# Kernel optimization log

Hardware: AMD Instinct MI355X
Metric: run time of the kernel (lower is better)

The kernel has to match this reference:

```python
import jax, jax.numpy as jnp
import numpy as np

N = 30000   # nodes
E = 480000  # edges
IN = 128    # hidden_dim (in_feats)
H = 4       # num_heads
D = 128     # out_feats per head
HD = H * D
NEG_SLOPE = 0.2
BN_EPS = 1e-5


def setup_inputs() -> dict:
    key = jax.random.key(0)
    ks = jax.random.split(key, 12)
    feat = jax.random.normal(ks[0], (N, IN), dtype=jnp.float32)
    src = jax.random.randint(ks[1], (E,), 0, N)
    dst = jax.random.randint(ks[2], (E,), 0, N)
    sc_in = 1.0 / np.sqrt(IN)
    sc_hd = 1.0 / np.sqrt(HD)
    W_fc = jax.random.normal(ks[3], (IN, HD), dtype=jnp.float32) * sc_in
    attn_l = jax.random.normal(ks[4], (H, D), dtype=jnp.float32) * sc_in
    attn_r = jax.random.normal(ks[5], (H, D), dtype=jnp.float32) * sc_in
    W_res = jax.random.normal(ks[6], (IN, HD), dtype=jnp.float32) * sc_in
    bias_gat = jnp.zeros((HD,), dtype=jnp.float32)
    gamma = jnp.ones((HD,), dtype=jnp.float32)
    beta = jnp.zeros((HD,), dtype=jnp.float32)
    W_out = jax.random.normal(ks[7], (HD, IN), dtype=jnp.float32) * sc_hd
    b_out = jnp.zeros((IN,), dtype=jnp.float32)
    return dict(feat=feat, src=src, dst=dst, W_fc=W_fc, attn_l=attn_l,
                attn_r=attn_r, W_res=W_res, bias_gat=bias_gat,
                gamma=gamma, beta=beta, W_out=W_out, b_out=b_out)


def reference(feat, src, dst, W_fc, attn_l, attn_r, W_res, bias_gat,
              gamma, beta, W_out, b_out):
    # --- GATConv (eval mode: dropout off) ---
    h = (feat @ W_fc).reshape(N, H, D)               # projected feats [N,H,D]
    el = jnp.einsum('nhd,hd->nh', h, attn_l)         # [N,H]
    er = jnp.einsum('nhd,hd->nh', h, attn_r)         # [N,H]
    e = el[src] + er[dst]                            # [E,H]
    e = jnp.where(e > 0, e, NEG_SLOPE * e)           # leaky_relu(0.2)
    # segment softmax over edges grouped by destination node
    emax = jax.ops.segment_max(e, dst, num_segments=N)   # [N,H]
    emax = jnp.where(jnp.isfinite(emax), emax, 0.0)      # empty segments
    ex = jnp.exp(e - emax[dst])                          # [E,H]
    denom = jax.ops.segment_sum(ex, dst, num_segments=N) # [N,H]
    a = ex / denom[dst]                                  # [E,H] attention
    msgs = h[src] * a[:, :, None]                        # [E,H,D]
    rst = jax.ops.segment_sum(msgs, dst, num_segments=N) # [N,H,D]
    # residual (in_feats != H*out_feats -> linear res_fc) + bias
    rst = rst + (feat @ W_res).reshape(N, H, D) + bias_gat.reshape(1, H, D)
    # --- fc_out: Flatten -> BatchNorm1d (train stats) -> ReLU -> Linear ---
    x = rst.reshape(N, HD)
    mu = x.mean(axis=0)
    var = x.var(axis=0)
    xn = (x - mu) / jnp.sqrt(var + BN_EPS)
    x = jnp.maximum(gamma * xn + beta, 0.0)
    return x @ W_out + b_out                             # [N, IN]
```

## Files before the change

### kernel.cpp

```cpp
#include <hip/hip_runtime.h>

#define N_  30000
#define E_  480000

typedef short short8 __attribute__((ext_vector_type(8)));
typedef float f32x4  __attribute__((ext_vector_type(4)));
typedef float f32x2  __attribute__((ext_vector_type(2)));
typedef unsigned int u32x4 __attribute__((ext_vector_type(4)));
typedef unsigned int u32x2 __attribute__((ext_vector_type(2)));
typedef int i32x4 __attribute__((ext_vector_type(4)));
union Frag { u32x4 q; short8 v; unsigned short us[8]; };

__device__ __forceinline__ float b2f(unsigned short u){
  union { unsigned int i; float f; } v; v.i = ((unsigned int)u) << 16; return v.f;
}
__device__ __forceinline__ float blo(unsigned int u){
  union { unsigned int i; float f; } v; v.i = u << 16; return v.f;
}
__device__ __forceinline__ float bhi(unsigned int u){
  union { unsigned int i; float f; } v; v.i = u & 0xffff0000u; return v.f;
}
__device__ __forceinline__ unsigned short f2b(float f){
  union { float f; unsigned int u; } v; v.f = f;
  unsigned int u = v.u;
  return (unsigned short)((u + 0x7fffu + ((u >> 16) & 1u)) >> 16);
}

__global__ void k_initconv(const float* __restrict__ Wfc, const float* __restrict__ Wres,
                           const float* __restrict__ Wout,
                           const float* __restrict__ al, const float* __restrict__ ar,
                           unsigned short* __restrict__ Wt2, unsigned short* __restrict__ WtOut,
                           float* __restrict__ P,
                           int* __restrict__ counts, int* __restrict__ cursor){
  int bx = blockIdx.x;
  if (bx >= 256){
    int idx = (bx - 256) * 256 + threadIdx.x;
    if (idx < 1024){
      int k = idx >> 3, q = idx & 7;
      int h = q & 3;
      const float* a = (q < 4) ? al : ar;
      const float* wr = Wfc + k * 512 + h * 128;
      const float* av = a + h * 128;
      float s = 0.f;
#pragma unroll 4
      for (int d = 0; d < 128; d++) s += wr[d] * av[d];
      P[k * 8 + q] = s;
    }
    return;
  }
  int gid = bx * 256 + threadIdx.x;
  const int stride = 256 * 256;
  if (gid < N_){ counts[gid] = 0; cursor[gid] = 0; }
  const int total1 = 512 * 256;
  const int total2 = 128 * 512;
  for (int i = gid; i < total1 + total2; i += stride){
    if (i < total1){
      int c = i >> 8, k = i & 255;
      float v = (k < 128) ? Wfc[k * 512 + c] : Wres[(k - 128) * 512 + c];
      Wt2[((k >> 7) << 16) + c * 128 + (k & 127)] = f2b(v);
    } else {
      int j = i - total1;
      int n = j >> 9, k = j & 511;
      WtOut[((k >> 7) << 14) + n * 128 + (k & 127)] = f2b(Wout[k * 128 + n]);
    }
  }
}

__global__ __launch_bounds__(256) void k_el(const float* __restrict__ feat,
                                            const float* __restrict__ P,
                                            float* __restrict__ el, float* __restrict__ er,
                                            unsigned short* __restrict__ featb){
  __shared__ float sF[32 * 132];
  __shared__ float sP[1024];
  int t = threadIdx.x;
  int n0 = blockIdx.x * 32;
  *reinterpret_cast<f32x4*>(&sP[t * 4]) = *reinterpret_cast<const f32x4*>(P + t * 4);
#pragma unroll
  for (int i = 0; i < 4; i++){
    int c = t + i * 256;
    int r = c >> 5, cw = (c & 31) * 4;
    int gn = n0 + r;
    f32x4 v = {0.f, 0.f, 0.f, 0.f};
    if (gn < N_) v = *reinterpret_cast<const f32x4*>(feat + gn * 128 + cw);
    *reinterpret_cast<f32x4*>(&sF[r * 132 + cw]) = v;
  }
  __syncthreads();
#pragma unroll
  for (int i = 0; i < 8; i++){
    int c = t + i * 256;
    int r = c >> 6, cw = (c & 63) * 2;
    int gn = n0 + r;
    if (gn < N_){
      float v0 = sF[r * 132 + cw], v1 = sF[r * 132 + cw + 1];
      unsigned int pv = (unsigned int)f2b(v0) | ((unsigned int)f2b(v1) << 16);
      *reinterpret_cast<unsigned int*>(featb + gn * 128 + cw) = pv;
    }
  }
  int node = t >> 3, q = t & 7;
  int gn = n0 + node;
  const float* fr = &sF[node * 132];
  float s = 0.f;
#pragma unroll 2
  for (int k = 0; k < 128; k += 4){
    f32x4 fv = *reinterpret_cast<const f32x4*>(fr + k);
#pragma unroll
    for (int j = 0; j < 4; j++) s += fv[j] * sP[(k + j) * 8 + q];
  }
  if (gn < N_){
    if (q < 4) el[gn * 4 + q] = s;
    else       er[gn * 4 + (q - 4)] = s;
  }
}

__global__ void k_hist(const int* __restrict__ dst, int* __restrict__ counts){
  int e = blockIdx.x * 256 + threadIdx.x;
  if (e < E_) atomicAdd(&counts[dst[e]], 1);
}

__global__ __launch_bounds__(1024) void k_scan(const int* __restrict__ counts,
                                               int* __restrict__ offs){
  __shared__ int wsum[16];
  int t = threadIdx.x;
  int lane = t & 63, w = t >> 6;
  int base = t * 32;
  int vals[32];
  int s = 0;
  bool inb = (base < N_);
#pragma unroll
  for (int jj = 0; jj < 8; jj++){
    i32x4 cv = {0, 0, 0, 0};
    if (inb) cv = *reinterpret_cast<const i32x4*>(counts + base + jj * 4);
#pragma unroll
    for (int m = 0; m < 4; m++){
      int idx = base + jj * 4 + m;
      int v = (idx < N_) ? cv[m] : 0;
      vals[jj * 4 + m] = s;
      s += v;
    }
  }
  int x = s;
  for (int o = 1; o < 64; o <<= 1){
    int y = __shfl_up(x, o);
    if (lane >= o) x += y;
  }
  if (lane == 63) wsum[w] = x;
  __syncthreads();
  if (t < 16){
    int y = wsum[t];
    for (int o = 1; o < 16; o <<= 1){
      int z = __shfl_up(y, o, 16);
      if (t >= o) y += z;
    }
    wsum[t] = y;
  }
  __syncthreads();
  int wbase = (w > 0) ? wsum[w - 1] : 0;
  int ex = wbase + x - s;
#pragma unroll
  for (int j = 0; j < 32; j++){
    int idx = base + j;
    if (idx <= N_) offs[idx] = ex + vals[j];
  }
}

__global__ void k_edge(const int* __restrict__ src, const int* __restrict__ dst,
                       const float* __restrict__ el, const float* __restrict__ er,
                       float* __restrict__ ws_s, int* __restrict__ src_s,
                       const int* __restrict__ offs, int* __restrict__ cursor){
  int e = blockIdx.x * 256 + threadIdx.x;
  if (e >= E_) return;
  int s = src[e], d = dst[e];
  f32x4 a = *reinterpret_cast<const f32x4*>(el + s * 4);
  f32x4 b = *reinterpret_cast<const f32x4*>(er + d * 4);
  f32x4 v;
#pragma unroll
  for (int i = 0; i < 4; i++){
    float x = a[i] + b[i];
    x = x > 0.f ? x : 0.2f * x;
    v[i] = __expf(x);
  }
  int p = atomicAdd(&cursor[d], 1);
  int pos = offs[d] + p;
  *reinterpret_cast<f32x4*>(ws_s + pos * 4) = v;
  src_s[pos] = s;
}

__global__ __launch_bounds__(256) void k_aggrf(const int* __restrict__ offs,
                                               const int* __restrict__ src_s,
                                               const float* __restrict__ ws_s,
                                               const unsigned short* __restrict__ featb,
                                               unsigned short* __restrict__ fagg){
  int wave = threadIdx.x >> 6, lane = threadIdx.x & 63;
  int n = blockIdx.x * 4 + wave;
  if (n >= N_) return;
  int off0 = __builtin_amdgcn_readfirstlane(offs[n]);
  int g    = __builtin_amdgcn_readfirstlane(offs[n + 1]) - off0;
  int c0 = lane * 2;
  f32x2 acc2[4] = {};
  f32x4 wsum = {0.f, 0.f, 0.f, 0.f};

  auto FMA1 = [&](const f32x4& wv, unsigned int pv){
    wsum += wv;
    f32x2 lh; lh[0] = blo(pv); lh[1] = bhi(pv);
#pragma unroll
    for (int h = 0; h < 4; h++) acc2[h] += lh * wv[h];
  };

  int i = 0;
  while (i < g){
    int blk = g - i; if (blk > 64) blk = 64;
    int idx = i + lane;
    int ssrc = (idx < g) ? src_s[off0 + idx] : 0;
    int nfull = blk >> 3;
    if (nfull){
      int sa[8]; unsigned int pa[8]; f32x4 wa[8];
#pragma unroll
      for (int u = 0; u < 8; u++) sa[u] = __shfl(ssrc, u);
#pragma unroll
      for (int u = 0; u < 8; u++) pa[u] = *reinterpret_cast<const unsigned int*>(featb + sa[u] * 128 + c0);
#pragma unroll
      for (int u = 0; u < 8; u++) wa[u] = *reinterpret_cast<const f32x4*>(ws_s + (off0 + i + u) * 4);
      for (int c = 1; c < nfull; c++){
        int sb[8]; unsigned int pb[8]; f32x4 wb[8];
#pragma unroll
        for (int u = 0; u < 8; u++) sb[u] = __shfl(ssrc, c * 8 + u);
#pragma unroll
        for (int u = 0; u < 8; u++) pb[u] = *reinterpret_cast<const unsigned int*>(featb + sb[u] * 128 + c0);
#pragma unroll
        for (int u = 0; u < 8; u++) wb[u] = *reinterpret_cast<const f32x4*>(ws_s + (off0 + i + c * 8 + u) * 4);
#pragma unroll
        for (int u = 0; u < 8; u++) FMA1(wa[u], pa[u]);
#pragma unroll
        for (int u = 0; u < 8; u++){ pa[u] = pb[u]; wa[u] = wb[u]; }
      }
#pragma unroll
      for (int u = 0; u < 8; u++) FMA1(wa[u], pa[u]);
    }
    for (int j = nfull * 8; j < blk; j++){
      int s = __shfl(ssrc, j);
      unsigned int pv = *reinterpret_cast<const unsigned int*>(featb + s * 128 + c0);
      f32x4 wv = *reinterpret_cast<const f32x4*>(ws_s + (off0 + i + j) * 4);
      FMA1(wv, pv);
    }
    i += blk;
  }

  f32x4 rd;
#pragma unroll
  for (int h = 0; h < 4; h++) rd[h] = (wsum[h] > 0.f) ? 1.0f / wsum[h] : 0.f;
#pragma unroll
  for (int h = 0; h < 4; h++){
    unsigned int ov = (unsigned int)f2b(acc2[h][0] * rd[h]) |
                      ((unsigned int)f2b(acc2[h][1] * rd[h]) << 16);
    *reinterpret_cast<unsigned int*>(fagg + n * 512 + h * 128 + c0) = ov;
  }
}

__global__ __launch_bounds__(512) void k_gemmC(const unsigned short* __restrict__ fagg,
                                               const unsigned short* __restrict__ featb,
                                               const unsigned short* __restrict__ Wt2,
                                               const float* __restrict__ bias,
                                               unsigned short* __restrict__ comb,
                                               float* __restrict__ psum,
                                               float* __restrict__ psq){
  __shared__ unsigned short wsl[256 * 128];
  char* wb = (char*)wsl;
  int tid = threadIdx.x;
  int wave = tid >> 6, lane = tid & 63;
  int lrow = lane & 15, quad = lane >> 4;
  int rowbase = blockIdx.x * 128 + wave * 16;
  int colbase = blockIdx.y * 256;
  int h0 = blockIdx.y * 2;
  int arow = rowbase + lrow; if (arow > N_ - 1) arow = N_ - 1;
  const unsigned short* aF = fagg + arow * 512 + h0 * 128;
  const unsigned short* aX = featb + arow * 128;
  f32x4 acc[16] = {};
  for (int phase = 0; phase < 2; phase++){
    __syncthreads();
#pragma unroll
    for (int i = 0; i < 8; i++){
      int c = tid + i * 512;
      int col = c >> 4, unit = c & 15;
      u32x4 v = *reinterpret_cast<const u32x4*>(Wt2 + (phase << 16) + (colbase + col) * 128 + unit * 8);
      int byte = (col * 256 + unit * 16) ^ ((col & 7) << 4);
      *reinterpret_cast<u32x4*>(wb + byte) = v;
    }
    __syncthreads();
#pragma unroll
    for (int kk = 0; kk < 4; kk++){
      Frag a0, a1;
      if (phase == 0){
        a0.q = *reinterpret_cast<const u32x4*>(aF + kk * 32 + quad * 8);
        a1.q = *reinterpret_cast<const u32x4*>(aF + 128 + kk * 32 + quad * 8);
      } else {
        a0.q = *reinterpret_cast<const u32x4*>(aX + kk * 32 + quad * 8);
        a1.q = a0.q;
      }
#pragma unroll
      for (int s = 0; s < 16; s++){
        int r = s * 16 + lrow;
        int byte = (r * 256 + kk * 64 + quad * 16) ^ ((r & 7) << 4);
        Frag b; b.q = *reinterpret_cast<const u32x4*>(wb + byte);
        acc[s] = __builtin_amdgcn_mfma_f32_16x16x32_bf16(b.v, (s < 8 ? a0.v : a1.v), acc[s], 0, 0, 0);
      }
    }
  }
  __syncthreads();
  float* psumL = (float*)wsl;
  float* psqL  = (float*)wsl + 2048;
  int gr = rowbase + lrow;
  bool valid = (gr < N_);
  unsigned short* crow = comb + gr * 512 + colbase;
#pragma unroll
  for (int s = 0; s < 16; s++){
    f32x4 bb = *reinterpret_cast<const f32x4*>(bias + colbase + s * 16 + quad * 4);
    f32x4 x, sv, qv;
#pragma unroll
    for (int j = 0; j < 4; j++){
      x[j] = acc[s][j] + bb[j];
      sv[j] = valid ? x[j] : 0.f;
      qv[j] = sv[j] * x[j];
    }
    if (valid){
      u32x2 ov;
#pragma unroll
      for (int d = 0; d < 2; d++)
        ov[d] = (unsigned int)f2b(x[2*d]) | ((unsigned int)f2b(x[2*d+1]) << 16);
      *reinterpret_cast<u32x2*>(crow + s * 16 + quad * 4) = ov;
    }
#pragma unroll
    for (int o = 8; o >= 1; o >>= 1){
#pragma unroll
      for (int j = 0; j < 4; j++){
        sv[j] += __shfl_xor(sv[j], o, 16);
        qv[j] += __shfl_xor(qv[j], o, 16);
      }
    }
    if (lrow == 0){
      int ch = s * 16 + quad * 4;
      *reinterpret_cast<f32x4*>(&psumL[wave * 256 + ch]) = sv;
      *reinterpret_cast<f32x4*>(&psqL [wave * 256 + ch]) = qv;
    }
  }
  __syncthreads();
  {
    int ch = tid & 255;
    const float* bufL = (tid < 256) ? psumL : psqL;
    float a = 0.f;
#pragma unroll
    for (int w2 = 0; w2 < 8; w2++) a += bufL[w2 * 256 + ch];
    float* gdst = (tid < 256) ? (psum + blockIdx.x * 512 + blockIdx.y * 256 + ch)
                              : (psq  + blockIdx.x * 512 + blockIdx.y * 256 + ch);
    *gdst = a;
  }
}

__global__ __launch_bounds__(128) void k_bnfin(const float* __restrict__ psum,
                                               const float* __restrict__ psq,
                                               const float* __restrict__ gamma,
                                               const float* __restrict__ beta,
                                               float* __restrict__ scale,
                                               float* __restrict__ shift){
  int ch = blockIdx.x * 128 + threadIdx.x;
  float sum = 0.f, sq = 0.f;
#pragma unroll 5
  for (int b = 0; b < 235; b++){
    sum += psum[b * 512 + ch];
    sq  += psq [b * 512 + ch];
  }
  float mu  = sum / (float)N_;
  float var = sq / (float)N_ - mu * mu;
  float inv = rsqrtf(var + 1e-5f);
  float sc  = gamma[ch] * inv;
  scale[ch] = sc;
  shift[ch] = beta[ch] - mu * sc;
}

__global__ __launch_bounds__(512) void k_gemm2(const unsigned short* __restrict__ comb,
                                               const unsigned short* __restrict__ WtOut,
                                               const float* __restrict__ scale,
                                               const float* __restrict__ shift,
                                               const float* __restrict__ bout,
                                               float* __restrict__ out){
  __shared__ float sc[512], sh[512];
  __shared__ unsigned short wsl[128 * 128];
  char* wb = (char*)wsl;
  int t = threadIdx.x;
  sc[t] = scale[t]; sh[t] = shift[t];
  int wave = t >> 6, lane = t & 63, lrow = lane & 15, quad = lane >> 4;
  int rowbase = blockIdx.x * 128 + wave * 16;
  int rr = rowbase + lrow; if (rr > N_ - 1) rr = N_ - 1;
  const unsigned short* arow = comb + rr * 512;
  f32x4 acc[8] = {};
  for (int phase = 0; phase < 4; phase++){
    __syncthreads();
#pragma unroll
    for (int i = 0; i < 4; i++){
      int c = t + i * 512;
      int col = c >> 4, unit = c & 15;
      u32x4 v = *reinterpret_cast<const u32x4*>(WtOut + (phase << 14) + col * 128 + unit * 8);
      int byte = (col * 256 + unit * 16) ^ ((col & 7) << 4);
      *reinterpret_cast<u32x4*>(wb + byte) = v;
    }
    __syncthreads();
#pragma unroll
    for (int kk = 0; kk < 4; kk++){
      int base = phase * 128 + kk * 32 + quad * 8;
      Frag a; a.q = *reinterpret_cast<const u32x4*>(arow + base);
#pragma unroll
      for (int i2 = 0; i2 < 8; i2++){
        float x = b2f(a.us[i2]);
        x = fmaf(x, sc[base + i2], sh[base + i2]);
        a.us[i2] = f2b(fmaxf(x, 0.0f));
      }
#pragma unroll
      for (int s = 0; s < 8; s++){
        int r = s * 16 + lrow;
        int byte = (r * 256 + kk * 64 + quad * 16) ^ ((r & 7) << 4);
        Frag b; b.q = *reinterpret_cast<const u32x4*>(wb + byte);
        acc[s] = __builtin_amdgcn_mfma_f32_16x16x32_bf16(b.v, a.v, acc[s], 0, 0, 0);
      }
    }
  }
  int gr = rowbase + lrow;
  if (gr < N_){
    float* orow = out + gr * 128;
#pragma unroll
    for (int s = 0; s < 8; s++){
      int cb = s * 16 + quad * 4;
      f32x4 bb = *reinterpret_cast<const f32x4*>(bout + cb);
      f32x4 ov;
#pragma unroll
      for (int j = 0; j < 4; j++) ov[j] = acc[s][j] + bb[j];
      *reinterpret_cast<f32x4*>(orow + cb) = ov;
    }
  }
}

extern "C" void kernel_launch(void* const* d_in, const int* in_sizes, int n_in,
                              void* d_out, int out_size, void* d_ws, size_t ws_size,
                              hipStream_t stream){
  const float* feat  = (const float*)d_in[0];
  const int*   src   = (const int*)d_in[1];
  const int*   dst   = (const int*)d_in[2];
  const float* Wfc   = (const float*)d_in[3];
  const float* al    = (const float*)d_in[4];
  const float* ar    = (const float*)d_in[5];
  const float* Wres  = (const float*)d_in[6];
  const float* bias  = (const float*)d_in[7];
  const float* gamma = (const float*)d_in[8];
  const float* beta  = (const float*)d_in[9];
  const float* Wout  = (const float*)d_in[10];
  const float* bout  = (const float*)d_in[11];
  float* out = (float*)d_out;

  char* ws = (char*)d_ws;
  unsigned short* comb  = (unsigned short*)(ws + 0);
  unsigned short* fagg  = (unsigned short*)(ws + 30720000);
  unsigned short* Wt2   = (unsigned short*)(ws + 61440000);
  unsigned short* WtOut = (unsigned short*)(ws + 61702144);
  float*          el    = (float*)(ws + 61833216);
  float*          er    = (float*)(ws + 62313216);
  float*          ws_s  = (float*)(ws + 62793216);
  int*            offs  = (int*)(ws + 70473216);
  int*            counts= (int*)(ws + 70593280);
  int*            cursor= (int*)(ws + 70713280);
  int*            src_s = (int*)(ws + 70833280);
  float*          psum  = (float*)(ws + 72753280);
  float*          psq   = (float*)(ws + 73277568);
  float*          scale = (float*)(ws + 73801856);
  float*          shift = (float*)(ws + 73803904);
  unsigned short* featb = (unsigned short*)(ws + 73805952);
  float*          P     = psum;

  k_initconv<<<260, 256, 0, stream>>>(Wfc, Wres, Wout, al, ar, Wt2, WtOut, P,
                                      counts, cursor);
  k_hist<<<(E_ + 255) / 256, 256, 0, stream>>>(dst, counts);
  k_scan<<<1, 1024, 0, stream>>>(counts, offs);
  k_el<<<(N_ + 31) / 32, 256, 0, stream>>>(feat, P, el, er, featb);
  k_edge<<<(E_ + 255) / 256, 256, 0, stream>>>(src, dst, el, er, ws_s, src_s, offs, cursor);
  k_aggrf<<<(N_ + 3) / 4, 256, 0, stream>>>(offs, src_s, ws_s, featb, fagg);
  dim3 gC((N_ + 127) / 128, 2);
  k_gemmC<<<gC, 512, 0, stream>>>(fagg, featb, Wt2, bias, comb, psum, psq);
  k_bnfin<<<4, 128, 0, stream>>>(psum, psq, gamma, beta, scale, shift);
  k_gemm2<<<(N_ + 127) / 128, 512, 0, stream>>>(comb, WtOut, scale, shift, bout, out);
}
```

Before: 277.2 us.

## Split BN statistics out of combined GEMM and retile GEMMs for more blocks

The combine GEMM now tiles 128 columns per block over a 4-wide grid, halving accumulators and LDS so more blocks run at once, and no longer computes BatchNorm partial sums. A separate k_stats kernel reads the bf16 combined output back to compute per-channel sums and squares across 256 blocks, and bnfin reduces these with four independent accumulators. The output GEMM moves to 256-thread, 64-row blocks to raise block count. The trade is an extra kernel launch plus a full reread of the combined matrix, and statistics are now taken from bf16-rounded values rather than fp32.

```diff
diff --git a/kernel.cpp b/kernel.cpp
--- a/kernel.cpp
+++ b/kernel.cpp
@@ -260,25 +260,22 @@
                                                const unsigned short* __restrict__ featb,
                                                const unsigned short* __restrict__ Wt2,
                                                const float* __restrict__ bias,
-                                               unsigned short* __restrict__ comb,
-                                               float* __restrict__ psum,
-                                               float* __restrict__ psq){
-  __shared__ unsigned short wsl[256 * 128];
+                                               unsigned short* __restrict__ comb){
+  __shared__ unsigned short wsl[128 * 128];
   char* wb = (char*)wsl;
   int tid = threadIdx.x;
   int wave = tid >> 6, lane = tid & 63;
   int lrow = lane & 15, quad = lane >> 4;
   int rowbase = blockIdx.x * 128 + wave * 16;
-  int colbase = blockIdx.y * 256;
-  int h0 = blockIdx.y * 2;
+  int colbase = blockIdx.y * 128;
   int arow = rowbase + lrow; if (arow > N_ - 1) arow = N_ - 1;
-  const unsigned short* aF = fagg + arow * 512 + h0 * 128;
+  const unsigned short* aF = fagg + arow * 512 + colbase;
   const unsigned short* aX = featb + arow * 128;
-  f32x4 acc[16] = {};
+  f32x4 acc[8] = {};
   for (int phase = 0; phase < 2; phase++){
     __syncthreads();
 #pragma unroll
-    for (int i = 0; i < 8; i++){
+    for (int i = 0; i < 4; i++){
       int c = tid + i * 512;
       int col = c >> 4, unit = c & 15;
       u32x4 v = *reinterpret_cast<const u32x4*>(Wt2 + (phase << 16) + (colbase + col) * 128 + unit * 8);
@@ -288,70 +285,68 @@
     __syncthreads();
 #pragma unroll
     for (int kk = 0; kk < 4; kk++){
-      Frag a0, a1;
-      if (phase == 0){
-        a0.q = *reinterpret_cast<const u32x4*>(aF + kk * 32 + quad * 8);
-        a1.q = *reinterpret_cast<const u32x4*>(aF + 128 + kk * 32 + quad * 8);
-      } else {
-        a0.q = *reinterpret_cast<const u32x4*>(aX + kk * 32 + quad * 8);
-        a1.q = a0.q;
-      }
-#pragma unroll
-      for (int s = 0; s < 16; s++){
+      Frag a;
+      a.q = (phase == 0)
+          ? *reinterpret_cast<const u32x4*>(aF + kk * 32 + quad * 8)
+          : *reinterpret_cast<const u32x4*>(aX + kk * 32 + quad * 8);
+#pragma unroll
+      for (int s = 0; s < 8; s++){
         int r = s * 16 + lrow;
         int byte = (r * 256 + kk * 64 + quad * 16) ^ ((r & 7) << 4);
         Frag b; b.q = *reinterpret_cast<const u32x4*>(wb + byte);
-        acc[s] = __builtin_amdgcn_mfma_f32_16x16x32_bf16(b.v, (s < 8 ? a0.v : a1.v), acc[s], 0, 0, 0);
+        acc[s] = __builtin_amdgcn_mfma_f32_16x16x32_bf16(b.v, a.v, acc[s], 0, 0, 0);
       }
     }
   }
+  int gr = rowbase + lrow;
+  if (gr < N_){
+    unsigned short* crow = comb + gr * 512 + colbase;
+#pragma unroll
+    for (int s = 0; s < 8; s++){
+      f32x4 bb = *reinterpret_cast<const f32x4*>(bias + colbase + s * 16 + quad * 4);
+      u32x2 ov;
+#pragma unroll
+      for (int d = 0; d < 2; d++){
+        float v0 = acc[s][2 * d]     + bb[2 * d];
+        float v1 = acc[s][2 * d + 1] + bb[2 * d + 1];
+        ov[d] = (unsigned int)f2b(v0) | ((unsigned int)f2b(v1) << 16);
+      }
+      *reinterpret_cast<u32x2*>(crow + s * 16 + quad * 4) = ov;
+    }
+  }
+}
+
+__global__ __launch_bounds__(256) void k_stats(const unsigned short* __restrict__ comb,
+                                               float* __restrict__ psum,
+                                               float* __restrict__ psq){
+  __shared__ float lsum[4][512];
+  __shared__ float lsq[4][512];
+  int t = threadIdx.x, lane = t & 63, rg = t >> 6;
+  int c0 = lane * 8;
+  const int rows = 118;
+  int r0 = blockIdx.x * rows;
+  int r1 = r0 + rows; if (r1 > N_) r1 = N_;
+  float s[8] = {}, q[8] = {};
+  for (int r = r0 + rg; r < r1; r += 4){
+    u32x4 pv = *reinterpret_cast<const u32x4*>(comb + r * 512 + c0);
+#pragma unroll
+    for (int d = 0; d < 4; d++){
+      float v0 = blo(pv[d]);
+      float v1 = bhi(pv[d]);
+      s[2*d]   += v0; q[2*d]   += v0 * v0;
+      s[2*d+1] += v1; q[2*d+1] += v1 * v1;
+    }
+  }
+#pragma unroll
+  for (int d = 0; d < 8; d++){ lsum[rg][c0 + d] = s[d]; lsq[rg][c0 + d] = q[d]; }
   __syncthreads();
-  float* psumL = (float*)wsl;
-  float* psqL  = (float*)wsl + 2048;
-  int gr = rowbase + lrow;
-  bool valid = (gr < N_);
-  unsigned short* crow = comb + gr * 512 + colbase;
-#pragma unroll
-  for (int s = 0; s < 16; s++){
-    f32x4 bb = *reinterpret_cast<const f32x4*>(bias + colbase + s * 16 + quad * 4);
-    f32x4 x, sv, qv;
-#pragma unroll
-    for (int j = 0; j < 4; j++){
-      x[j] = acc[s][j] + bb[j];
-      sv[j] = valid ? x[j] : 0.f;
-      qv[j] = sv[j] * x[j];
-    }
-    if (valid){
-      u32x2 ov;
-#pragma unroll
-      for (int d = 0; d < 2; d++)
-        ov[d] = (unsigned int)f2b(x[2*d]) | ((unsigned int)f2b(x[2*d+1]) << 16);
-      *reinterpret_cast<u32x2*>(crow + s * 16 + quad * 4) = ov;
-    }
-#pragma unroll
-    for (int o = 8; o >= 1; o >>= 1){
-#pragma unroll
-      for (int j = 0; j < 4; j++){
-        sv[j] += __shfl_xor(sv[j], o, 16);
-        qv[j] += __shfl_xor(qv[j], o, 16);
-      }
-    }
-    if (lrow == 0){
-      int ch = s * 16 + quad * 4;
-      *reinterpret_cast<f32x4*>(&psumL[wave * 256 + ch]) = sv;
-      *reinterpret_cast<f32x4*>(&psqL [wave * 256 + ch]) = qv;
-    }
-  }
-  __syncthreads();
-  {
-    int ch = tid & 255;
-    const float* bufL = (tid < 256) ? psumL : psqL;
-    float a = 0.f;
-#pragma unroll
-    for (int w2 = 0; w2 < 8; w2++) a += bufL[w2 * 256 + ch];
-    float* gdst = (tid < 256) ? (psum + blockIdx.x * 512 + blockIdx.y * 256 + ch)
-                              : (psq  + blockIdx.x * 512 + blockIdx.y * 256 + ch);
-    *gdst = a;
+#pragma unroll
+  for (int half = 0; half < 2; half++){
+    int ch = t + half * 256;
+    float a = lsum[0][ch] + lsum[1][ch] + lsum[2][ch] + lsum[3][ch];
+    float b = lsq[0][ch] + lsq[1][ch] + lsq[2][ch] + lsq[3][ch];
+    psum[blockIdx.x * 512 + ch] = a;
+    psq[blockIdx.x * 512 + ch] = b;
   }
 }
 
@@ -362,12 +357,20 @@
                                                float* __restrict__ scale,
                                                float* __restrict__ shift){
   int ch = blockIdx.x * 128 + threadIdx.x;
-  float sum = 0.f, sq = 0.f;
-#pragma unroll 5
-  for (int b = 0; b < 235; b++){
-    sum += psum[b * 512 + ch];
-    sq  += psq [b * 512 + ch];
-  }
+  float s0 = 0.f, s1 = 0.f, s2 = 0.f, s3 = 0.f;
+  float q0 = 0.f, q1 = 0.f, q2 = 0.f, q3 = 0.f;
+  for (int b = 0; b < 256; b += 4){
+    s0 += psum[(b    ) * 512 + ch];
+    s1 += psum[(b + 1) * 512 + ch];
+    s2 += psum[(b + 2) * 512 + ch];
+    s3 += psum[(b + 3) * 512 + ch];
+    q0 += psq[(b    ) * 512 + ch];
+    q1 += psq[(b + 1) * 512 + ch];
+    q2 += psq[(b + 2) * 512 + ch];
+    q3 += psq[(b + 3) * 512 + ch];
+  }
+  float sum = (s0 + s1) + (s2 + s3);
+  float sq  = (q0 + q1) + (q2 + q3);
   float mu  = sum / (float)N_;
   float var = sq / (float)N_ - mu * mu;
   float inv = rsqrtf(var + 1e-5f);
@@ -376,7 +379,7 @@
   shift[ch] = beta[ch] - mu * sc;
 }
 
-__global__ __launch_bounds__(512) void k_gemm2(const unsigned short* __restrict__ comb,
+__global__ __launch_bounds__(256) void k_gemm2(const unsigned short* __restrict__ comb,
                                                const unsigned short* __restrict__ WtOut,
                                                const float* __restrict__ scale,
                                                const float* __restrict__ shift,
@@ -386,17 +389,17 @@
   __shared__ unsigned short wsl[128 * 128];
   char* wb = (char*)wsl;
   int t = threadIdx.x;
-  sc[t] = scale[t]; sh[t] = shift[t];
+  for (int i = t; i < 512; i += 256){ sc[i] = scale[i]; sh[i] = shift[i]; }
   int wave = t >> 6, lane = t & 63, lrow = lane & 15, quad = lane >> 4;
-  int rowbase = blockIdx.x * 128 + wave * 16;
+  int rowbase = blockIdx.x * 64 + wave * 16;
   int rr = rowbase + lrow; if (rr > N_ - 1) rr = N_ - 1;
   const unsigned short* arow = comb + rr * 512;
   f32x4 acc[8] = {};
   for (int phase = 0; phase < 4; phase++){
     __syncthreads();
 #pragma unroll
-    for (int i = 0; i < 4; i++){
-      int c = t + i * 512;
+    for (int i = 0; i < 8; i++){
+      int c = t + i * 256;
       int col = c >> 4, unit = c & 15;
       u32x4 v = *reinterpret_cast<const u32x4*>(WtOut + (phase << 14) + col * 128 + unit * 8);
       int byte = (col * 256 + unit * 16) ^ ((col & 7) << 4);
@@ -480,8 +483,9 @@
   k_el<<<(N_ + 31) / 32, 256, 0, stream>>>(feat, P, el, er, featb);
   k_edge<<<(E_ + 255) / 256, 256, 0, stream>>>(src, dst, el, er, ws_s, src_s, offs, cursor);
   k_aggrf<<<(N_ + 3) / 4, 256, 0, stream>>>(offs, src_s, ws_s, featb, fagg);
-  dim3 gC((N_ + 127) / 128, 2);
-  k_gemmC<<<gC, 512, 0, stream>>>(fagg, featb, Wt2, bias, comb, psum, psq);
+  dim3 gC((N_ + 127) / 128, 4);
+  k_gemmC<<<gC, 512, 0, stream>>>(fagg, featb, Wt2, bias, comb);
+  k_stats<<<256, 256, 0, stream>>>(comb, psum, psq);
   k_bnfin<<<4, 128, 0, stream>>>(psum, psq, gamma, beta, scale, shift);
-  k_gemm2<<<(N_ + 127) / 128, 512, 0, stream>>>(comb, WtOut, scale, shift, bout, out);
-}
+  k_gemm2<<<(N_ + 63) / 64, 256, 0, stream>>>(comb, WtOut, scale, shift, bout, out);
+}
```

New measurement: 265.4 us. -4.3%, faster.
